# Kernel tuning notes

Measured on AMD Instinct MI355X. Metric: run time of the kernel, lower is better.

Reference implementation:

```python
import jax, jax.numpy as jnp
import numpy as np

T, B, D_MODEL, D_KEY = 4096, 4, 1024, 1024


def setup_inputs() -> dict:
    key = jax.random.key(0)
    kx, kq, kk, kv = jax.random.split(key, 4)
    scale = 1.0 / np.sqrt(D_MODEL)
    x = jax.random.normal(kx, (T, B, D_MODEL), dtype=jnp.float32)
    # torch.nn.Linear weights are [out_features, in_features]
    Wq = jax.random.uniform(kq, (D_KEY, D_MODEL), dtype=jnp.float32, minval=-scale, maxval=scale)
    Wk = jax.random.uniform(kk, (D_KEY, D_MODEL), dtype=jnp.float32, minval=-scale, maxval=scale)
    Wv = jax.random.uniform(kv, (D_MODEL, D_MODEL), dtype=jnp.float32, minval=-scale, maxval=scale)
    return {"x": x, "Wq": Wq, "Wk": Wk, "Wv": Wv}


def _kernel(u):
    return jax.nn.elu(u) + 1.0


def reference(x, Wq, Wk, Wv):
    # x: [T, B, d_model] (time-major, as in the original module)
    Q = _kernel(jnp.einsum('tbd,kd->tbk', x, Wq))  # [T, B, d_key]
    K = _kernel(jnp.einsum('tbd,kd->tbk', x, Wk))  # [T, B, d_key]
    V = jnp.einsum('tbd,md->tbm', x, Wv)           # [T, B, d_model]

    s0 = jnp.zeros((D_KEY, D_MODEL), dtype=x.dtype)  # shared state: sums K^T V over time AND batch
    z0 = jnp.zeros((B, D_KEY), dtype=x.dtype)        # per-batch normalizer state

    def step(carry, qkv):
        s, z = carry
        q, k, v = qkv                                  # q,k: [B, d_key]; v: [B, d_model]
        s = s + jnp.einsum('bk,bm->km', k, v)          # [d_key, d_model] (sums over batch, per original)
        z = z + k                                      # [B, d_key]
        numer = q @ s                                  # [B, d_model]
        denom = jnp.sum(q * z, axis=-1, keepdims=True) # [B, 1]
        return (s, z), numer / denom

    _, y = jax.lax.scan(step, (s0, z0), (Q, K, V))
    return y  # [T, B, d_model]
```

## Files before the change

kernel.cpp:

```cpp
#include <hip/hip_runtime.h>
#include <hip/hip_bf16.h>
#include <stdint.h>

typedef unsigned short u16;
typedef __attribute__((ext_vector_type(8))) __bf16 bf16x8;
typedef __attribute__((ext_vector_type(4))) float floatx4;
typedef __attribute__((ext_vector_type(8))) unsigned short us8;
typedef __attribute__((ext_vector_type(4))) unsigned short us4;

#define TT 4096
#define BB 4
#define DM 1024
#define ROWS (TT * BB)
#define CHUNK 128
#define CR (CHUNK * BB)
#define NC (TT / CHUNK)
#define MB (1024l * 1024l)

__device__ __forceinline__ float b2f(u16 x) {
  union { unsigned int u; float f; } v; v.u = ((unsigned int)x) << 16; return v.f;
}
__device__ __forceinline__ u16 f2b(float f) {
  union { float f; unsigned int u; } v; v.f = f;
  unsigned int r = v.u + 0x7fffu + ((v.u >> 16) & 1u);
  return (u16)(r >> 16);
}

__global__ void k_sniff(const u16* __restrict__ x, int* __restrict__ flag) {
  const int lane = threadIdx.x & 63;
  int cnt = 0;
#pragma unroll
  for (int k = 0; k < 32; ++k) {
    u16 u = x[2 * (lane + 64 * k)];
    int e = (u >> 7) & 0xFF;
    cnt += (e >= 100 && e <= 140) ? 1 : 0;
  }
#pragma unroll
  for (int d = 32; d > 0; d >>= 1) cnt += __shfl_down(cnt, d, 64);
  if (lane == 0) *flag = (cnt >= 1024) ? 1 : 0;
}

__global__ __launch_bounds__(256) void k_convert(const void* __restrict__ src,
                                                 u16* __restrict__ dst,
                                                 const int* __restrict__ flag, long n) {
  long i = ((long)blockIdx.x * 256 + threadIdx.x) * 4;
  if (i >= n) return;
  if (*flag) {
    *(us4*)(dst + i) = *(const us4*)((const u16*)src + i);
  } else {
    const float* s = (const float*)src;
    us4 o;
#pragma unroll
    for (int e = 0; e < 4; ++e) o[e] = f2b(s[i + e]);
    *(us4*)(dst + i) = o;
  }
}

__device__ __forceinline__ void ldsg16(const u16* g, u16* l) {
  auto gp = reinterpret_cast<__attribute__((address_space(1))) void*>(
      reinterpret_cast<uintptr_t>(const_cast<u16*>(g)));
  auto lp = reinterpret_cast<__attribute__((address_space(3))) void*>(
      (unsigned int)reinterpret_cast<uintptr_t>(l));
  __builtin_amdgcn_global_load_lds(gp, lp, 16, 0, 0);
}

__device__ __forceinline__ void bar() {
  asm volatile("" ::: "memory");
  __builtin_amdgcn_s_barrier();
  asm volatile("" ::: "memory");
}
__device__ __forceinline__ void vm0() {
  asm volatile("s_waitcnt vmcnt(0)" ::: "memory");
}
__device__ __forceinline__ void stage4(const u16* g, u16* l, long s64) {
  ldsg16(g, l);
  ldsg16(g + s64, l + 4096);
  ldsg16(g + 2 * s64, l + 8192);
  ldsg16(g + 3 * s64, l + 12288);
}

#define LDA4(OFF) \
  _Pragma("unroll") \
  for (int mi = 0; mi < 4; ++mi) af[mi] = *(const bf16x8*)(pA + mi * 2048 + (OFF))

#define MFMA16(AC0, BF) \
  _Pragma("unroll") \
  for (int mi = 0; mi < 4; ++mi) \
    _Pragma("unroll") \
    for (int ni = 0; ni < 4; ++ni) \
      acc[(AC0) + mi][ni] = __builtin_amdgcn_mfma_f32_16x16x32_bf16(af[mi], BF[ni], acc[(AC0) + mi][ni], 0, 0, 0)

__device__ __forceinline__ void gemm256(
    const u16* __restrict__ A, long lda,
    const u16* __restrict__ B, long ldb,
    int K, u16* sA, u16* sB, floatx4 acc[8][4])
{
  const int t = threadIdx.x, w = t >> 6, lane = t & 63;
  const int quad = lane >> 4, m16 = lane & 15;
  const int wm = w >> 2, wn = w & 3;
  const int csw = ((t & 7) ^ ((t >> 4) & 7)) << 3;
  const u16* ga = A + (long)(t >> 3) * lda + csw;
  const u16* gb = B + (long)(t >> 3) * ldb + csw;
  const long a64 = 64l * lda, b64 = 64l * ldb;
  u16* lA = sA + w * 512;
  u16* lB = sB + w * 512;
  const char* cA = (const char*)sA;
  const char* cB = (const char*)sB;
  const int lx = ((m16 >> 1) & 7) << 4;
  const int raB = (wm * 128 + m16) << 7;
  const int rbB = (wn * 64 + m16) << 7;
  const int kq0 = (quad << 4) ^ lx;
  const int kq1 = (64 + (quad << 4)) ^ lx;
  const int NT = K >> 6;

  stage4(ga, lA, a64);
  stage4(gb, lB, b64);
  vm0();
  bar();

  for (int kt = 0; kt < NT; ++kt) {
    const char* pA = cA + ((kt & 1) << 15) + raB;
    const char* pB = cB + ((kt & 1) << 15) + rbB;
    const bool pf = (kt + 1 < NT);
    const long ko = (long)(kt + 1) << 6;
    const int d1 = ((kt + 1) & 1) << 14;
    bf16x8 af[4], bf0[4], bf1[4];

    LDA4(kq0);
#pragma unroll
    for (int ni = 0; ni < 4; ++ni) bf0[ni] = *(const bf16x8*)(pB + ni * 2048 + kq0);
    if (pf) stage4(ga + ko, lA + d1, a64);
    bar();
    __builtin_amdgcn_s_setprio(1);
    MFMA16(0, bf0);
    __builtin_amdgcn_s_setprio(0);
    bar();

    LDA4(kq1);
#pragma unroll
    for (int ni = 0; ni < 4; ++ni) bf1[ni] = *(const bf16x8*)(pB + ni * 2048 + kq1);
    if (pf) stage4(gb + ko, lB + d1, b64);
    bar();
    __builtin_amdgcn_s_setprio(1);
    MFMA16(0, bf1);
    __builtin_amdgcn_s_setprio(0);
    bar();

    LDA4(8192 + kq0);
    bar();
    __builtin_amdgcn_s_setprio(1);
    MFMA16(4, bf0);
    __builtin_amdgcn_s_setprio(0);
    bar();

    LDA4(8192 + kq1);
    bar();
    __builtin_amdgcn_s_setprio(1);
    MFMA16(4, bf1);
    __builtin_amdgcn_s_setprio(0);
    if (pf) vm0();
    bar();
  }
}

__device__ __forceinline__ void gemm128(
    const u16* __restrict__ A, long lda,
    const u16* __restrict__ B, long ldb,
    int K, u16* sA, u16* sB, floatx4 acc[4][4])
{
  const int t = threadIdx.x, w = t >> 6, lane = t & 63;
  const int m16 = lane & 15, quad = lane >> 4;
  const int wm = w >> 1, wn = w & 1;
  const int sq = (lane & 3) ^ ((lane >> 3) & 3);
  const u16* ga = A + (long)(t >> 2) * lda + sq * 8;
  const u16* gb = B + (long)(t >> 2) * ldb + sq * 8;
  const long a64 = 64l * lda, b64 = 64l * ldb;
  u16* lA = sA + w * 512;
  u16* lB = sB + w * 512;
  const char* cA = (const char*)sA;
  const char* cB = (const char*)sB;
  const int slot = quad ^ ((m16 >> 1) & 3);
  const int aoff = wm * 4096 + m16 * 64 + slot * 16;
  const int boff = wn * 4096 + m16 * 64 + slot * 16;
  for (int k0 = 0; k0 < K; k0 += 32) {
    __syncthreads();
    ldsg16(ga, lA);
    ldsg16(ga + a64, lA + 2048);
    ldsg16(gb, lB);
    ldsg16(gb + b64, lB + 2048);
    ga += 32; gb += 32;
    __syncthreads();
    bf16x8 af[4], bfr[4];
#pragma unroll
    for (int i = 0; i < 4; ++i) af[i]  = *(const bf16x8*)(cA + aoff + i * 1024);
#pragma unroll
    for (int i = 0; i < 4; ++i) bfr[i] = *(const bf16x8*)(cB + boff + i * 1024);
#pragma unroll
    for (int im = 0; im < 4; ++im)
#pragma unroll
      for (int in = 0; in < 4; ++in)
        acc[im][in] = __builtin_amdgcn_mfma_f32_16x16x32_bf16(af[im], bfr[in], acc[im][in], 0, 0, 0);
  }
}

__global__ __launch_bounds__(512, 2) void k_proj2(
    const u16* __restrict__ X, const u16* __restrict__ Wt, u16* __restrict__ Y, int mode)
{
  __shared__ __align__(16) u16 sm[65536];
  floatx4 acc[8][4] = {};
  const int id = blockIdx.x;
  const int m0 = (id >> 2) * 256, n0 = (id & 3) * 256;
  gemm256(X + (long)m0 * DM, DM, Wt + (long)n0 * DM, DM, DM, sm, sm + 32768, acc);
  const int t = threadIdx.x, w = t >> 6, lane = t & 63;
  const int wm = w >> 2, wn = w & 3, quad = lane >> 4, c16 = lane & 15;
#pragma unroll
  for (int mi = 0; mi < 8; ++mi)
#pragma unroll
    for (int ni = 0; ni < 4; ++ni) {
      const int gr = m0 + wm * 128 + mi * 16 + quad * 4;
      const int gc = n0 + wn * 64 + ni * 16 + c16;
      floatx4 v = acc[mi][ni];
      if (mode == 2) {
        us4 o;
#pragma unroll
        for (int e = 0; e < 4; ++e) o[e] = f2b(v[e]);
        *(us4*)(Y + (long)gc * ROWS + gr) = o;
      } else {
#pragma unroll
        for (int e = 0; e < 4; ++e) {
          float u = v[e];
          u = u > 0.f ? u + 1.f : __expf(u);
          Y[(long)(gr + e) * DM + gc] = f2b(u);
        }
      }
    }
}

__global__ __launch_bounds__(256) void k_transpose(const u16* __restrict__ src, u16* __restrict__ dst)
{
  const int t = threadIdx.x;
  const int sx = t & 15, sy = t >> 4;
  const long r0 = (long)blockIdx.x * 128 + sy * 8;
  const long c0 = (long)blockIdx.y * 128 + sx * 8;
  us8 r[8];
#pragma unroll
  for (int v = 0; v < 8; ++v) r[v] = *(const us8*)(src + (r0 + v) * DM + c0);
#pragma unroll
  for (int u = 0; u < 8; ++u) {
    us8 o;
#pragma unroll
    for (int v = 0; v < 8; ++v) o[v] = r[v][u];
    *(us8*)(dst + (c0 + u) * ROWS + r0) = o;
  }
}

__global__ __launch_bounds__(256) void k_cksum(const u16* __restrict__ Kp, float* __restrict__ cs)
{
  const int id = blockIdx.x * 256 + threadIdx.x;
  const int i = id & 1023, b = (id >> 10) & 3, j = id >> 12;
  const u16* p = Kp + ((long)j * CR + b) * DM + i;
  float a = 0.f;
#pragma unroll 8
  for (int tl = 0; tl < CHUNK; ++tl) a += b2f(p[(long)tl * BB * DM]);
  cs[id] = a;
}

__global__ __launch_bounds__(256) void k_zfill(const u16* __restrict__ Kp,
                                               const float* __restrict__ cs,
                                               u16* __restrict__ z)
{
  const int id = blockIdx.x * 256 + threadIdx.x;
  const int i = id & 1023, b = (id >> 10) & 3, j = id >> 12;
  float a = 0.f;
  for (int j2 = 0; j2 < j; ++j2) a += cs[j2 * 4096 + b * 1024 + i];
  const u16* p = Kp + ((long)j * CR + b) * DM + i;
  u16* q = z + ((long)j * CR + b) * DM + i;
  for (int tl = 0; tl < CHUNK; ++tl) {
    a += b2f(p[(long)tl * BB * DM]);
    q[(long)tl * BB * DM] = f2b(a);
  }
}

__global__ __launch_bounds__(512, 2) void k_gemm_g2(
    const u16* __restrict__ Vt, const u16* __restrict__ Kt, u16* __restrict__ G)
{
  __shared__ __align__(16) u16 sm[65536];
  floatx4 acc[8][4] = {};
  const int id = blockIdx.x;
  const int x = id & 7, s = id >> 3;
  const int j = x + 8 * (s >> 4);
  const int nm = s & 15;
  const int n0 = (nm & 3) * 256;
  const int m0 = (nm >> 2) * 256;
  gemm256(Vt + (long)m0 * ROWS + j * CR, ROWS,
          Kt + (long)n0 * ROWS + j * CR, ROWS, CR, sm, sm + 32768, acc);
  const int t = threadIdx.x, w = t >> 6, lane = t & 63;
  const int wm = w >> 2, wn = w & 3, quad = lane >> 4, c16 = lane & 15;
  u16* Gj = G + (long)j * DM * DM;
#pragma unroll
  for (int mi = 0; mi < 8; ++mi)
#pragma unroll
    for (int ni = 0; ni < 4; ++ni) {
      const int gr = m0 + wm * 128 + mi * 16 + quad * 4;
      const int gc = n0 + wn * 64 + ni * 16 + c16;
      floatx4 v = acc[mi][ni];
#pragma unroll
      for (int e = 0; e < 4; ++e) Gj[(long)(gr + e) * DM + gc] = f2b(v[e]);
    }
}

__global__ __launch_bounds__(256) void k_prefix(u16* __restrict__ G)
{
  const long id = (long)blockIdx.x * 256 + threadIdx.x;
  float a = 0.f;
#pragma unroll
  for (int j = 0; j < NC; ++j) {
    u16* p = G + (long)j * DM * DM + id;
    float g = b2f(*p);
    *p = f2b(a);
    a += g;
  }
}

__global__ __launch_bounds__(256) void k_scores(
    const u16* __restrict__ Q, const u16* __restrict__ Kp, u16* __restrict__ P)
{
  __shared__ __align__(16) u16 sA[4096];
  __shared__ __align__(16) u16 sB[4096];
  floatx4 acc[4][4] = {};
  const int id = blockIdx.x;
  const int x = id & 7, s = id >> 3;
  const int j = x + 8 * (s >> 4);
  const int nm = s & 15;
  const int n0 = (nm & 3) * 128;
  const int m0 = (nm >> 2) * 128;
  if (n0 <= m0) {
    gemm128(Q + ((long)j * CR + m0) * DM, DM,
            Kp + ((long)j * CR + n0) * DM, DM, DM, sA, sB, acc);
  }
  const int t = threadIdx.x, lane = t & 63, w = t >> 6;
  const int wm = w >> 1, wn = w & 1, quad = lane >> 4, c16 = lane & 15;
  u16* Pj = P + (long)j * CR * CR;
#pragma unroll
  for (int im = 0; im < 4; ++im)
#pragma unroll
    for (int in = 0; in < 4; ++in) {
      const int gc = n0 + wn * 64 + in * 16 + c16;
      const int gr = m0 + wm * 64 + im * 16 + quad * 4;
      const bool valid = (gc <= gr + 3);
      floatx4 v = acc[im][in];
#pragma unroll
      for (int e = 0; e < 4; ++e)
        Pj[(long)(gr + e) * CR + gc] = valid ? f2b(v[e]) : (u16)0;
    }
}

__global__ __launch_bounds__(256) void k_denom(
    const u16* __restrict__ Q, const u16* __restrict__ z, float* __restrict__ denom)
{
  const int w = threadIdx.x >> 6, lane = threadIdx.x & 63;
  const long row = (long)blockIdx.x * 4 + w;
  const u16* q = Q + row * DM;
  const u16* zz = z + row * DM;
  float s = 0.f;
#pragma unroll
  for (int p = 0; p < 2; ++p) {
    const int off = lane * 8 + p * 512;
    us8 q8 = *(const us8*)(q + off);
    us8 z8 = *(const us8*)(zz + off);
#pragma unroll
    for (int e = 0; e < 8; ++e) s += b2f(q8[e]) * b2f(z8[e]);
  }
#pragma unroll
  for (int d = 32; d > 0; d >>= 1) s += __shfl_down(s, d, 64);
  if (lane == 0) denom[row] = s;
}

__global__ __launch_bounds__(512, 2) void k_out2(
    const u16* __restrict__ P, const u16* __restrict__ Vt,
    const u16* __restrict__ Q, const u16* __restrict__ St,
    const float* __restrict__ denom, void* __restrict__ out,
    const int* __restrict__ flag)
{
  __shared__ __align__(16) u16 sm[65536];
  floatx4 acc[8][4] = {};
  const int id = blockIdx.x;
  const int x = id & 7, s = id >> 3;
  const int j = x + 8 * (s >> 3);
  const int nm = s & 7;
  const int n0 = (nm & 3) * 256;
  const int m0 = (nm >> 2) * 256;
  gemm256(P + (long)j * CR * CR + (long)m0 * CR, CR,
          Vt + (long)n0 * ROWS + j * CR, ROWS, m0 + 256, sm, sm + 32768, acc);
  gemm256(Q + ((long)j * CR + m0) * DM, DM,
          St + (long)j * DM * DM + (long)n0 * DM, DM, DM, sm, sm + 32768, acc);
  const int t = threadIdx.x, w = t >> 6, lane = t & 63;
  const int wm = w >> 2, wn = w & 3, quad = lane >> 4, c16 = lane & 15;
  const int isf16 = *flag;
  float* of = (float*)out;
  u16* ob = (u16*)out;
#pragma unroll
  for (int mi = 0; mi < 8; ++mi)
#pragma unroll
    for (int ni = 0; ni < 4; ++ni) {
      const int gc = n0 + wn * 64 + ni * 16 + c16;
      const int grl = m0 + wm * 128 + mi * 16 + quad * 4;
      const long gr = (long)j * CR + grl;
      floatx4 v = acc[mi][ni];
#pragma unroll
      for (int e = 0; e < 4; ++e) {
        const float d = denom[gr + e];
        const float y = v[e] / d;
        if (isf16) ob[(gr + e) * DM + gc] = f2b(y);
        else       of[(gr + e) * DM + gc] = y;
      }
    }
}

extern "C" void kernel_launch(void* const* d_in, const int* in_sizes, int n_in,
                              void* d_out, int out_size, void* d_ws, size_t ws_size,
                              hipStream_t stream)
{
  char* ws = (char*)d_ws;
  u16*  xc  = (u16*)(ws);
  u16*  z   = (u16*)(ws);
  u16*  Q   = (u16*)(ws + 32 * MB);
  u16*  K   = (u16*)(ws + 64 * MB);
  u16*  Kt  = (u16*)(ws + 96 * MB);
  u16*  P   = (u16*)(ws + 96 * MB);
  u16*  Vt  = (u16*)(ws + 128 * MB);
  u16*  G   = (u16*)(ws + 160 * MB);
  u16*  Wqc = (u16*)(ws + 224 * MB);
  u16*  Wkc = (u16*)(ws + 226 * MB);
  u16*  Wvc = (u16*)(ws + 228 * MB);
  float* cs = (float*)(ws + 230 * MB);
  float* dn = (float*)(ws + 230 * MB + 524288);
  int* flag = (int*)(ws + 230 * MB + 524288 + 65536);

  dim3 blk(256), blk5(512);
  k_sniff<<<1, 64, 0, stream>>>((const u16*)d_in[0], flag);
  k_convert<<<16384, blk, 0, stream>>>(d_in[0], xc, flag, (long)ROWS * DM);
  k_convert<<<1024, blk, 0, stream>>>(d_in[1], Wqc, flag, (long)DM * DM);
  k_convert<<<1024, blk, 0, stream>>>(d_in[2], Wkc, flag, (long)DM * DM);
  k_convert<<<1024, blk, 0, stream>>>(d_in[3], Wvc, flag, (long)DM * DM);
  k_proj2<<<dim3(256), blk5, 0, stream>>>(xc, Wqc, Q, 1);
  k_proj2<<<dim3(256), blk5, 0, stream>>>(xc, Wkc, K, 1);
  k_proj2<<<dim3(256), blk5, 0, stream>>>(xc, Wvc, Vt, 2);
  k_transpose<<<dim3(128, 8), blk, 0, stream>>>(K, Kt);
  k_cksum<<<dim3(512), blk, 0, stream>>>(K, cs);
  k_zfill<<<dim3(512), blk, 0, stream>>>(K, cs, z);
  k_gemm_g2<<<dim3(512), blk5, 0, stream>>>(Vt, Kt, G);
  k_prefix<<<dim3(4096), blk, 0, stream>>>(G);
  k_scores<<<dim3(512), blk, 0, stream>>>(Q, K, P);
  k_denom<<<dim3(4096), blk, 0, stream>>>(Q, z, dn);
  k_out2<<<dim3(256), blk5, 0, stream>>>(P, Vt, Q, G, dn, d_out, flag);
}
```

Measured before the change: 441.1 us.

## Deepen GEMM prefetch to two tiles ahead and chain two GEMMs in one pipeline

The 256x256 GEMM core now issues global-to-LDS loads two K-tiles ahead, waiting with vmcnt(8) instead of draining all loads every iteration. Loads are issued after the last LDS read of the current buffer, protected by an lgkmcnt wait and sched barriers. A combined two-GEMM variant lets k_out2 run its P*V and Q*S products as one continuous pipeline without a drain between them. The projection kernel also remaps block IDs for better cache locality. The trade-off is tighter ordering requirements on LDS buffer reuse, which could cause hazards if the waits are wrong.

After: 448.2 us. About the same (+1.6%).

```diff
diff --git a/kernel.cpp b/kernel.cpp
--- a/kernel.cpp
+++ b/kernel.cpp
@@ -69,9 +69,6 @@
   __builtin_amdgcn_s_barrier();
   asm volatile("" ::: "memory");
 }
-__device__ __forceinline__ void vm0() {
-  asm volatile("s_waitcnt vmcnt(0)" ::: "memory");
-}
 __device__ __forceinline__ void stage4(const u16* g, u16* l, long s64) {
   ldsg16(g, l);
   ldsg16(g + s64, l + 4096);
@@ -90,18 +87,24 @@
     for (int ni = 0; ni < 4; ++ni) \
       acc[(AC0) + mi][ni] = __builtin_amdgcn_mfma_f32_16x16x32_bf16(af[mi], BF[ni], acc[(AC0) + mi][ni], 0, 0, 0)
 
-__device__ __forceinline__ void gemm256(
-    const u16* __restrict__ A, long lda,
-    const u16* __restrict__ B, long ldb,
-    int K, u16* sA, u16* sB, floatx4 acc[8][4])
+__device__ __forceinline__ void gemm256s(
+    const u16* __restrict__ A1, long lda1,
+    const u16* __restrict__ B1, long ldb1, int K1,
+    const u16* __restrict__ A2, long lda2,
+    const u16* __restrict__ B2, long ldb2, int K2,
+    u16* sA, u16* sB, floatx4 acc[8][4])
 {
   const int t = threadIdx.x, w = t >> 6, lane = t & 63;
   const int quad = lane >> 4, m16 = lane & 15;
   const int wm = w >> 2, wn = w & 3;
   const int csw = ((t & 7) ^ ((t >> 4) & 7)) << 3;
-  const u16* ga = A + (long)(t >> 3) * lda + csw;
-  const u16* gb = B + (long)(t >> 3) * ldb + csw;
-  const long a64 = 64l * lda, b64 = 64l * ldb;
+  const long row = t >> 3;
+  const u16* ga1 = A1 + row * lda1 + csw;
+  const u16* gb1 = B1 + row * ldb1 + csw;
+  const u16* ga2 = A2 + row * lda2 + csw;
+  const u16* gb2 = B2 + row * ldb2 + csw;
+  const long a641 = 64l * lda1, b641 = 64l * ldb1;
+  const long a642 = 64l * lda2, b642 = 64l * ldb2;
   u16* lA = sA + w * 512;
   u16* lB = sB + w * 512;
   const char* cA = (const char*)sA;
@@ -111,25 +114,29 @@
   const int rbB = (wn * 64 + m16) << 7;
   const int kq0 = (quad << 4) ^ lx;
   const int kq1 = (64 + (quad << 4)) ^ lx;
-  const int NT = K >> 6;
-
-  stage4(ga, lA, a64);
-  stage4(gb, lB, b64);
-  vm0();
+  const int NT1 = K1 >> 6, NT = (K1 + K2) >> 6;
+
+  auto STAGE = [&](int tt, int buf) {
+    const u16 *sa, *sb; long s64a, s64b;
+    if (tt < NT1) { sa = ga1 + (long)tt * 64;         sb = gb1 + (long)tt * 64;         s64a = a641; s64b = b641; }
+    else          { long u = tt - NT1; sa = ga2 + u * 64; sb = gb2 + u * 64;            s64a = a642; s64b = b642; }
+    stage4(sa, lA + (buf << 14), s64a);
+    stage4(sb, lB + (buf << 14), s64b);
+  };
+
+  STAGE(0, 0);
+  STAGE(1, 1);
+  asm volatile("s_waitcnt vmcnt(8)" ::: "memory");
   bar();
 
   for (int kt = 0; kt < NT; ++kt) {
     const char* pA = cA + ((kt & 1) << 15) + raB;
     const char* pB = cB + ((kt & 1) << 15) + rbB;
-    const bool pf = (kt + 1 < NT);
-    const long ko = (long)(kt + 1) << 6;
-    const int d1 = ((kt + 1) & 1) << 14;
     bf16x8 af[4], bf0[4], bf1[4];
 
     LDA4(kq0);
 #pragma unroll
     for (int ni = 0; ni < 4; ++ni) bf0[ni] = *(const bf16x8*)(pB + ni * 2048 + kq0);
-    if (pf) stage4(ga + ko, lA + d1, a64);
     bar();
     __builtin_amdgcn_s_setprio(1);
     MFMA16(0, bf0);
@@ -139,7 +146,6 @@
     LDA4(kq1);
 #pragma unroll
     for (int ni = 0; ni < 4; ++ni) bf1[ni] = *(const bf16x8*)(pB + ni * 2048 + kq1);
-    if (pf) stage4(gb + ko, lB + d1, b64);
     bar();
     __builtin_amdgcn_s_setprio(1);
     MFMA16(0, bf1);
@@ -154,11 +160,17 @@
     bar();
 
     LDA4(8192 + kq1);
-    bar();
+    asm volatile("s_waitcnt lgkmcnt(0)" ::: "memory");
+    __builtin_amdgcn_sched_barrier(0);
+    bar();
+    __builtin_amdgcn_sched_barrier(0);
+    if (kt + 2 < NT) STAGE(kt + 2, kt & 1);
     __builtin_amdgcn_s_setprio(1);
     MFMA16(4, bf1);
     __builtin_amdgcn_s_setprio(0);
-    if (pf) vm0();
+    __builtin_amdgcn_sched_barrier(0);
+    if (kt + 2 < NT)      { asm volatile("s_waitcnt vmcnt(8)" ::: "memory"); }
+    else if (kt + 1 < NT) { asm volatile("s_waitcnt vmcnt(0)" ::: "memory"); }
     bar();
   }
 }
@@ -208,9 +220,11 @@
 {
   __shared__ __align__(16) u16 sm[65536];
   floatx4 acc[8][4] = {};
-  const int id = blockIdx.x;
+  const int raw = blockIdx.x;
+  const int id = ((raw & 7) << 5) | (raw >> 3);
   const int m0 = (id >> 2) * 256, n0 = (id & 3) * 256;
-  gemm256(X + (long)m0 * DM, DM, Wt + (long)n0 * DM, DM, DM, sm, sm + 32768, acc);
+  gemm256s(X + (long)m0 * DM, DM, Wt + (long)n0 * DM, DM, DM,
+           X, DM, Wt, DM, 0, sm, sm + 32768, acc);
   const int t = threadIdx.x, w = t >> 6, lane = t & 63;
   const int wm = w >> 2, wn = w & 3, quad = lane >> 4, c16 = lane & 15;
 #pragma unroll
@@ -292,8 +306,9 @@
   const int nm = s & 15;
   const int n0 = (nm & 3) * 256;
   const int m0 = (nm >> 2) * 256;
-  gemm256(Vt + (long)m0 * ROWS + j * CR, ROWS,
-          Kt + (long)n0 * ROWS + j * CR, ROWS, CR, sm, sm + 32768, acc);
+  gemm256s(Vt + (long)m0 * ROWS + j * CR, ROWS,
+           Kt + (long)n0 * ROWS + j * CR, ROWS, CR,
+           Vt, ROWS, Kt, ROWS, 0, sm, sm + 32768, acc);
   const int t = threadIdx.x, w = t >> 6, lane = t & 63;
   const int wm = w >> 2, wn = w & 3, quad = lane >> 4, c16 = lane & 15;
   u16* Gj = G + (long)j * DM * DM;
@@ -390,10 +405,11 @@
   const int nm = s & 7;
   const int n0 = (nm & 3) * 256;
   const int m0 = (nm >> 2) * 256;
-  gemm256(P + (long)j * CR * CR + (long)m0 * CR, CR,
-          Vt + (long)n0 * ROWS + j * CR, ROWS, m0 + 256, sm, sm + 32768, acc);
-  gemm256(Q + ((long)j * CR + m0) * DM, DM,
-          St + (long)j * DM * DM + (long)n0 * DM, DM, DM, sm, sm + 32768, acc);
+  gemm256s(P + (long)j * CR * CR + (long)m0 * CR, CR,
+           Vt + (long)n0 * ROWS + j * CR, ROWS, m0 + 256,
+           Q + ((long)j * CR + m0) * DM, DM,
+           St + (long)j * DM * DM + (long)n0 * DM, DM, DM,
+           sm, sm + 32768, acc);
   const int t = threadIdx.x, w = t >> 6, lane = t & 63;
   const int wm = w >> 2, wn = w & 3, quad = lane >> 4, c16 = lane & 15;
   const int isf16 = *flag;
```
